# Performance work log

Hardware: AMD Instinct MI355X
Metric: run time of the kernel (lower is better)

## Reference

```python
import jax, jax.numpy as jnp
import numpy as np

D_NODE, D_PAIR, H = 512, 128, 16
HD = D_NODE // H  # head_dim = 32
B, N = 2, 1024


def _layernorm(x, gamma, beta, eps=1e-5):
    mu = jnp.mean(x, axis=-1, keepdims=True)
    var = jnp.var(x, axis=-1, keepdims=True)
    return (x - mu) * jax.lax.rsqrt(var + eps) * gamma + beta


def setup_inputs() -> dict:
    key = jax.random.key(0)
    ks = jax.random.split(key, 16)
    sc = 0.02
    inp = {
        's': jax.random.normal(ks[0], (B, N, D_NODE), jnp.float32),
        'z': jax.random.normal(ks[1], (B, N, N, D_PAIR), jnp.float32),
        'key_mask': jax.random.randint(ks[2], (B, N), 0, 2).astype(bool),
        'Wq': jax.random.normal(ks[3], (D_NODE, D_NODE), jnp.float32) * sc,
        'bq': jnp.zeros((D_NODE,), jnp.float32),
        'Wk': jax.random.normal(ks[4], (D_NODE, D_NODE), jnp.float32) * sc,
        'bk': jnp.zeros((D_NODE,), jnp.float32),
        'Wv': jax.random.normal(ks[5], (D_NODE, D_NODE), jnp.float32) * sc,
        'bv': jnp.zeros((D_NODE,), jnp.float32),
        'Wb': jax.random.normal(ks[6], (D_PAIR, H), jnp.float32) * sc,
        'bb': jnp.zeros((H,), jnp.float32),
        'Wg': jax.random.normal(ks[7], (D_NODE, D_NODE), jnp.float32) * sc,
        'bg': jnp.zeros((D_NODE,), jnp.float32),
        'Wo': jax.random.normal(ks[8], (D_NODE, D_NODE), jnp.float32) * sc,
        'bo': jnp.zeros((D_NODE,), jnp.float32),
        'gamma': jnp.ones((D_NODE,), jnp.float32),
        'beta': jnp.zeros((D_NODE,), jnp.float32),
    }
    return inp


def reference(s, z, key_mask, Wq, bq, Wk, bk, Wv, bv, Wb, bb, Wg, bg, Wo, bo, gamma, beta):
    b, n, _ = s.shape
    sn = _layernorm(s, gamma, beta)
    q = (sn @ Wq + bq).reshape(b, n, H, HD)
    k = (sn @ Wk + bk).reshape(b, n, H, HD)
    v = (sn @ Wv + bv).reshape(b, n, H, HD)
    # scores: [B, N(query), N(key), H]
    scores = jnp.einsum('bnhd,bmhd->bnmh', q, k) / np.sqrt(HD).astype(np.float32)
    scores = scores + (z @ Wb + bb)  # additive pair bias
    # mask keys (dim 2); True = masked out
    scores = jnp.where(key_mask[:, None, :, None], -jnp.inf, scores)
    attn = jax.nn.softmax(scores, axis=2)
    attn = jnp.nan_to_num(attn, nan=0.0)
    out = jnp.einsum('bnmh,bmhd->bnhd', attn, v).reshape(b, n, D_NODE)
    gate = jax.nn.sigmoid(sn @ Wg + bg)
    return gate * (out @ Wo + bo)
```

## Files before the change

### kernel.cpp

```cpp
#include <hip/hip_runtime.h>
#include <hip/hip_fp16.h>

typedef __attribute__((ext_vector_type(8))) _Float16 f16x8;
typedef __attribute__((ext_vector_type(8))) unsigned short u16x8;
typedef __attribute__((ext_vector_type(4))) float f32x4;

#define DEV __device__ __forceinline__

DEV unsigned short f2h(float f) {
  _Float16 h = (_Float16)f;
  return __builtin_bit_cast(unsigned short, h);
}
DEV float h2f(unsigned short u) {
  return (float)__builtin_bit_cast(_Float16, u);
}
DEV unsigned pk(float lo, float hi) {
  return (unsigned)f2h(lo) | ((unsigned)f2h(hi) << 16);
}

__global__ __launch_bounds__(256) void k_prep(const float* __restrict__ W0, const float* __restrict__ W1,
                                              const float* __restrict__ W2, const float* __restrict__ W3,
                                              const float* __restrict__ W4,
                                              unsigned short* __restrict__ T0, unsigned short* __restrict__ T1,
                                              unsigned short* __restrict__ T2, unsigned short* __restrict__ T3,
                                              unsigned short* __restrict__ T4,
                                              const unsigned* __restrict__ raw, int* __restrict__ canon) {
  int mat = blockIdx.y;
  const float* W = (mat == 0) ? W0 : (mat == 1) ? W1 : (mat == 2) ? W2 : (mat == 3) ? W3 : W4;
  unsigned short* T = (mat == 0) ? T0 : (mat == 1) ? T1 : (mat == 2) ? T2 : (mat == 3) ? T3 : T4;
  int tx = blockIdx.x & 7, ty = blockIdx.x >> 3;
  __shared__ float tile[64][65];
  int t = threadIdx.x;
  int r = t >> 6, c = t & 63;
#pragma unroll
  for (int i = 0; i < 16; ++i)
    tile[r + i * 4][c] = W[(size_t)(ty * 64 + r + i * 4) * 512 + tx * 64 + c];
  __syncthreads();
#pragma unroll
  for (int i = 0; i < 16; ++i)
    T[(size_t)(tx * 64 + r + i * 4) * 512 + ty * 64 + c] = f2h(tile[c][r + i * 4]);

  if (mat == 0 && blockIdx.x == 0) {
    __shared__ int s_gt1, s_f32;
    if (t == 0) { s_gt1 = 0; s_f32 = 0; }
    __syncthreads();
    int gt1 = 0, fv = 0;
    for (int i = t; i < 512; i += 256) {
      unsigned v = raw[i];
      if (v == 0x3F800000u) fv = 1;
      else if (v > 1u) gt1 = 1;
    }
    if (gt1) s_gt1 = 1;
    if (fv)  s_f32 = 1;
    __syncthreads();
    int mode = s_gt1 ? 1 : (s_f32 ? 2 : 0);
    for (int i = t; i < 2048; i += 256) {
      int v;
      if (mode == 1)      v = ((const unsigned char*)raw)[i] ? 1 : 0;
      else if (mode == 2) v = (((const float*)raw)[i] != 0.f) ? 1 : 0;
      else                v = raw[i] ? 1 : 0;
      canon[i] = v;
    }
  }
}

__global__ __launch_bounds__(64) void k_ln(const float* __restrict__ s,
                                           const float* __restrict__ gamma,
                                           const float* __restrict__ beta,
                                           unsigned short* __restrict__ sn) {
  int row = blockIdx.x, l = threadIdx.x;
  const float* sr = s + (size_t)row * 512 + l * 8;
  float4 x0 = *(const float4*)sr, x1 = *(const float4*)(sr + 4);
  float sum = x0.x + x0.y + x0.z + x0.w + x1.x + x1.y + x1.z + x1.w;
  float sq  = x0.x*x0.x + x0.y*x0.y + x0.z*x0.z + x0.w*x0.w
            + x1.x*x1.x + x1.y*x1.y + x1.z*x1.z + x1.w*x1.w;
#pragma unroll
  for (int off = 32; off >= 1; off >>= 1) {
    sum += __shfl_xor(sum, off);
    sq  += __shfl_xor(sq, off);
  }
  float mu = sum * (1.f / 512.f);
  float rstd = rsqrtf(sq * (1.f / 512.f) - mu * mu + 1e-5f);
  float4 g0 = *(const float4*)(gamma + l * 8), g1 = *(const float4*)(gamma + l * 8 + 4);
  float4 b0 = *(const float4*)(beta + l * 8),  b1 = *(const float4*)(beta + l * 8 + 4);
  u16x8 o;
  o[0] = f2h((x0.x - mu) * rstd * g0.x + b0.x);
  o[1] = f2h((x0.y - mu) * rstd * g0.y + b0.y);
  o[2] = f2h((x0.z - mu) * rstd * g0.z + b0.z);
  o[3] = f2h((x0.w - mu) * rstd * g0.w + b0.w);
  o[4] = f2h((x1.x - mu) * rstd * g1.x + b1.x);
  o[5] = f2h((x1.y - mu) * rstd * g1.y + b1.y);
  o[6] = f2h((x1.z - mu) * rstd * g1.z + b1.z);
  o[7] = f2h((x1.w - mu) * rstd * g1.w + b1.w);
  *(u16x8*)(sn + (size_t)row * 512 + l * 8) = o;
}

DEV void gemm_direct(const unsigned short* __restrict__ A,
                     const unsigned short* __restrict__ Wt,
                     const float* __restrict__ bvec,
                     void* __restrict__ outp,
                     const float* __restrict__ gate,
                     int mode, int ct, int rt) {
  int t = threadIdx.x, l = t & 63, w = t >> 6;
  int lane15 = l & 15, g = l >> 4;
  int wr = w >> 1, wc = w & 1;
  const unsigned short* ap[4];
  const unsigned short* bp[2];
#pragma unroll
  for (int mt = 0; mt < 4; ++mt)
    ap[mt] = A + (size_t)(rt * 128 + wr * 64 + mt * 16 + lane15) * 512 + g * 8;
#pragma unroll
  for (int nt = 0; nt < 2; ++nt)
    bp[nt] = Wt + (size_t)(ct * 64 + wc * 32 + nt * 16 + lane15) * 512 + g * 8;

  f32x4 acc[4][2];
#pragma unroll
  for (int mt = 0; mt < 4; ++mt)
#pragma unroll
    for (int nt = 0; nt < 2; ++nt) acc[mt][nt] = (f32x4){0.f, 0.f, 0.f, 0.f};

  f16x8 af[4], bf[2];
#pragma unroll
  for (int mt = 0; mt < 4; ++mt) af[mt] = *(const f16x8*)ap[mt];
#pragma unroll
  for (int nt = 0; nt < 2; ++nt) bf[nt] = *(const f16x8*)bp[nt];

  for (int ks = 0; ks < 16; ++ks) {
    f16x8 an[4], bn[2];
    if (ks < 15) {
#pragma unroll
      for (int mt = 0; mt < 4; ++mt) an[mt] = *(const f16x8*)(ap[mt] + (ks + 1) * 32);
#pragma unroll
      for (int nt = 0; nt < 2; ++nt) bn[nt] = *(const f16x8*)(bp[nt] + (ks + 1) * 32);
    } else {
#pragma unroll
      for (int mt = 0; mt < 4; ++mt) an[mt] = af[mt];
#pragma unroll
      for (int nt = 0; nt < 2; ++nt) bn[nt] = bf[nt];
    }
#pragma unroll
    for (int mt = 0; mt < 4; ++mt)
#pragma unroll
      for (int nt = 0; nt < 2; ++nt)
        acc[mt][nt] = __builtin_amdgcn_mfma_f32_16x16x32_f16(af[mt], bf[nt], acc[mt][nt], 0, 0, 0);
#pragma unroll
    for (int mt = 0; mt < 4; ++mt) af[mt] = an[mt];
#pragma unroll
    for (int nt = 0; nt < 2; ++nt) bf[nt] = bn[nt];
  }

#pragma unroll
  for (int mt = 0; mt < 4; ++mt)
#pragma unroll
    for (int nt = 0; nt < 2; ++nt) {
      int col = ct * 64 + wc * 32 + nt * 16 + lane15;
      float bv = bvec[col];
#pragma unroll
      for (int i = 0; i < 4; ++i) {
        int row = rt * 128 + wr * 64 + mt * 16 + g * 4 + i;
        float val = acc[mt][nt][i] + bv;
        int bb_ = row >> 10, n = row & 1023, hh = col >> 5, d = col & 31;
        if (mode == 0) {
          ((unsigned short*)outp)[(size_t)row * 512 + col] = f2h(val);
        } else if (mode == 1) {
          ((unsigned short*)outp)[(((size_t)bb_ * 16 + hh) * 1024 + n) * 32 + d] = f2h(val);
        } else if (mode == 2) {
          ((unsigned short*)outp)[(((size_t)bb_ * 16 + hh) * 32 + d) * 1024 + n] = f2h(val);
        } else if (mode == 3) {
          ((float*)outp)[(size_t)row * 512 + col] = 1.f / (1.f + __expf(-val));
        } else {
          ((float*)outp)[(size_t)row * 512 + col] = gate[(size_t)row * 512 + col] * val;
        }
      }
    }
}

__global__ __launch_bounds__(256) void k_qkvg(const unsigned short* __restrict__ A,
                                              const unsigned short* __restrict__ T0, const unsigned short* __restrict__ T1,
                                              const unsigned short* __restrict__ T2, const unsigned short* __restrict__ T3,
                                              const float* __restrict__ b0, const float* __restrict__ b1,
                                              const float* __restrict__ b2, const float* __restrict__ b3,
                                              void* o0, void* o1, void* o2, void* o3) {
  int mode = blockIdx.z;
  const unsigned short* Wt = (mode == 0) ? T0 : (mode == 1) ? T1 : (mode == 2) ? T2 : T3;
  const float* bv = (mode == 0) ? b0 : (mode == 1) ? b1 : (mode == 2) ? b2 : b3;
  void* o = (mode == 0) ? o0 : (mode == 1) ? o1 : (mode == 2) ? o2 : o3;
  gemm_direct(A, Wt, bv, o, nullptr, mode, blockIdx.x, blockIdx.y);
}

__global__ __launch_bounds__(256) void k_gemm_out(const unsigned short* __restrict__ A,
                                                  const unsigned short* __restrict__ Wt,
                                                  const float* __restrict__ bvec,
                                                  float* __restrict__ outp,
                                                  const float* __restrict__ gate) {
  gemm_direct(A, Wt, bvec, outp, gate, 4, blockIdx.x, blockIdx.y);
}

__global__ __launch_bounds__(256, 4) void k_bias(const float* __restrict__ z,
                                                 const float* __restrict__ Wb,
                                                 const float* __restrict__ bbp,
                                                 const int* __restrict__ maskc,
                                                 unsigned short* __restrict__ bias) {
  int bid = blockIdx.x;
  int slab = bid >> 1, half = bid & 1;
  int b = slab >> 10;
  int t = threadIdx.x, l = t & 63, w = t >> 6;
  int lane15 = l & 15, g = l >> 4;

  __shared__ float lds_[4][2048];
  float* wlds = lds_[w];

  f16x8 wf[4];
#pragma unroll
  for (int ks = 0; ks < 4; ++ks)
#pragma unroll
    for (int j = 0; j < 8; ++j)
      wf[ks][j] = (_Float16)Wb[(ks * 32 + g * 8 + j) * 16 + lane15];
  float bbh = bbp[lane15];

  const char* zb = (const char*)(z + ((size_t)slab * 1024 + half * 512 + (size_t)w * 128) * 128);
  unsigned short* ob = bias + ((size_t)slab * 16 + lane15) * 1024;
  const int* mrow = maskc + b * 1024;

  float4 rbuf[8];
#pragma unroll
  for (int i = 0; i < 8; ++i)
    rbuf[i] = *(const float4*)(zb + i * 1024 + l * 16);
#pragma unroll
  for (int i = 0; i < 8; ++i) {
    int lin = i * 1024 + l * 16;
    int off = lin ^ (((lin >> 9) & 7) << 4);
    *(float4*)((char*)wlds + off) = rbuf[i];
  }

  for (int t8 = 0; t8 < 8; ++t8) {
    if (t8 < 7) {
      const char* tb = zb + (t8 + 1) * 8192;
#pragma unroll
      for (int i = 0; i < 8; ++i)
        rbuf[i] = *(const float4*)(tb + i * 1024 + l * 16);
    }
    f32x4 acc = (f32x4){0.f, 0.f, 0.f, 0.f};
#pragma unroll
    for (int ks = 0; ks < 4; ++ks) {
      int linA = lane15 * 512 + ks * 128 + g * 32;
      int swz = ((lane15 & 7) << 4);
      float4 z0 = *(const float4*)((const char*)wlds + (linA ^ swz));
      float4 z1 = *(const float4*)((const char*)wlds + ((linA + 16) ^ swz));
      f16x8 af;
      af[0] = (_Float16)z0.x; af[1] = (_Float16)z0.y;
      af[2] = (_Float16)z0.z; af[3] = (_Float16)z0.w;
      af[4] = (_Float16)z1.x; af[5] = (_Float16)z1.y;
      af[6] = (_Float16)z1.z; af[7] = (_Float16)z1.w;
      acc = __builtin_amdgcn_mfma_f32_16x16x32_f16(af, wf[ks], acc, 0, 0, 0);
    }
    int mabs = half * 512 + w * 128 + t8 * 16 + 4 * g;
    int4 mk = *(const int4*)(mrow + mabs);
    ushort4 o4;
    o4.x = mk.x ? 0xFBFFu : f2h(acc[0] + bbh);
    o4.y = mk.y ? 0xFBFFu : f2h(acc[1] + bbh);
    o4.z = mk.z ? 0xFBFFu : f2h(acc[2] + bbh);
    o4.w = mk.w ? 0xFBFFu : f2h(acc[3] + bbh);
    *(ushort4*)(ob + mabs) = o4;
    if (t8 < 7) {
#pragma unroll
      for (int i = 0; i < 8; ++i) {
        int lin = i * 1024 + l * 16;
        int off = lin ^ (((lin >> 9) & 7) << 4);
        *(float4*)((char*)wlds + off) = rbuf[i];
      }
    }
  }
}

struct Pf {
  f16x8 kf1, kf2, vf1, vf2;
  ushort4 bv1, bv2;
};
DEV Pf ldchunk(const unsigned short* kb_, const unsigned short* vb_,
               const unsigned short* brow, int lane15, int g, int c) {
  Pf p;
  int m0 = c * 32;
  p.kf1 = *(const f16x8*)(kb_ + (size_t)(m0 + lane15) * 32 + g * 8);
  p.kf2 = *(const f16x8*)(kb_ + (size_t)(m0 + 16 + lane15) * 32 + g * 8);
  p.bv1 = *(const ushort4*)(brow + m0 + 4 * g);
  p.bv2 = *(const ushort4*)(brow + m0 + 16 + 4 * g);
  p.vf1 = *(const f16x8*)(vb_ + (size_t)lane15 * 1024 + m0 + 8 * g);
  p.vf2 = *(const f16x8*)(vb_ + (size_t)(16 + lane15) * 1024 + m0 + 8 * g);
  return p;
}

__global__ __launch_bounds__(512, 4) void k_attn(const unsigned short* __restrict__ qbuf,
                                                 const unsigned short* __restrict__ kbuf,
                                                 const unsigned short* __restrict__ vbuf,
                                                 const unsigned short* __restrict__ bias,
                                                 unsigned short* __restrict__ aout) {
  int qt = blockIdx.x, h = blockIdx.y, b = blockIdx.z;
  int t = threadIdx.x, l = t & 63, w = t >> 6;
  int qs = w & 3, half = w >> 2;
  int q0 = (qt * 4 + qs) * 16;
  int lane15 = l & 15, g = l >> 4;
  int bh = b * 16 + h;
  const float RS = 0.17677669529663687f;

  __shared__ float red_m[4][64];
  __shared__ float red_l[4][64];
  __shared__ f32x4 red_a1[4][64];
  __shared__ f32x4 red_a2[4][64];

  f16x8 qf = *(const f16x8*)(qbuf + ((size_t)(b * 1024 + q0 + lane15)) * 512 + h * 32 + g * 8);

  const unsigned short* kb_ = kbuf + (size_t)bh * 1024 * 32 + (size_t)half * 512 * 32;
  const unsigned short* vb_ = vbuf + (size_t)bh * 32 * 1024 + half * 512;
  const unsigned short* brow = bias + ((size_t)(b * 1024 + q0 + lane15) * 16 + h) * 1024 + half * 512;

  float m_run = -3.0e38f, lsum = 0.f;
  f32x4 acc1 = (f32x4){0.f, 0.f, 0.f, 0.f};
  f32x4 acc2 = (f32x4){0.f, 0.f, 0.f, 0.f};

  Pf cur = ldchunk(kb_, vb_, brow, lane15, g, 0);

  for (int c = 0; c < 16; ++c) {
    Pf nxt = cur;
    if (c < 15) nxt = ldchunk(kb_, vb_, brow, lane15, g, c + 1);

    f32x4 zero = (f32x4){0.f, 0.f, 0.f, 0.f};
    f32x4 c1 = __builtin_amdgcn_mfma_f32_16x16x32_f16(cur.kf1, qf, zero, 0, 0, 0);
    f32x4 c2 = __builtin_amdgcn_mfma_f32_16x16x32_f16(cur.kf2, qf, zero, 0, 0, 0);
    float s1[4], s2[4];
    s1[0] = c1[0] * RS + h2f(cur.bv1.x); s1[1] = c1[1] * RS + h2f(cur.bv1.y);
    s1[2] = c1[2] * RS + h2f(cur.bv1.z); s1[3] = c1[3] * RS + h2f(cur.bv1.w);
    s2[0] = c2[0] * RS + h2f(cur.bv2.x); s2[1] = c2[1] * RS + h2f(cur.bv2.y);
    s2[2] = c2[2] * RS + h2f(cur.bv2.z); s2[3] = c2[3] * RS + h2f(cur.bv2.w);
    float cm = fmaxf(fmaxf(fmaxf(s1[0], s1[1]), fmaxf(s1[2], s1[3])),
                     fmaxf(fmaxf(s2[0], s2[1]), fmaxf(s2[2], s2[3])));
    cm = fmaxf(cm, __shfl_xor(cm, 16));
    cm = fmaxf(cm, __shfl_xor(cm, 32));
    float mn = fmaxf(m_run, cm);
    float corr = __expf(m_run - mn);
    m_run = mn;
    float p1[4], p2[4], csum = 0.f;
#pragma unroll
    for (int i = 0; i < 4; ++i) { p1[i] = __expf(s1[i] - mn); csum += p1[i]; }
#pragma unroll
    for (int i = 0; i < 4; ++i) { p2[i] = __expf(s2[i] - mn); csum += p2[i]; }
    lsum = lsum * corr + csum;
#pragma unroll
    for (int i = 0; i < 4; ++i) { acc1[i] *= corr; acc2[i] *= corr; }
    unsigned a0 = pk(p1[0], p1[1]), a1 = pk(p1[2], p1[3]);
    unsigned b0 = pk(p2[0], p2[1]), b1 = pk(p2[2], p2[3]);
    int s0 = ((g & 1) << 5) + lane15, s1l = s0 + 16;
    unsigned wA0 = (unsigned)__shfl((int)a0, s0);
    unsigned wA1 = (unsigned)__shfl((int)a1, s0);
    unsigned wA2 = (unsigned)__shfl((int)a0, s1l);
    unsigned wA3 = (unsigned)__shfl((int)a1, s1l);
    unsigned wB0 = (unsigned)__shfl((int)b0, s0);
    unsigned wB1 = (unsigned)__shfl((int)b1, s0);
    unsigned wB2 = (unsigned)__shfl((int)b0, s1l);
    unsigned wB3 = (unsigned)__shfl((int)b1, s1l);
    bool hi = (l & 32) != 0;
    union { unsigned u[4]; f16x8 v; } pu;
    pu.u[0] = hi ? wB0 : wA0;
    pu.u[1] = hi ? wB1 : wA1;
    pu.u[2] = hi ? wB2 : wA2;
    pu.u[3] = hi ? wB3 : wA3;
    acc1 = __builtin_amdgcn_mfma_f32_16x16x32_f16(cur.vf1, pu.v, acc1, 0, 0, 0);
    acc2 = __builtin_amdgcn_mfma_f32_16x16x32_f16(cur.vf2, pu.v, acc2, 0, 0, 0);
    cur = nxt;
  }

  lsum += __shfl_xor(lsum, 16);
  lsum += __shfl_xor(lsum, 32);

  if (half) {
    red_m[qs][l] = m_run;
    red_l[qs][l] = lsum;
    red_a1[qs][l] = acc1;
    red_a2[qs][l] = acc2;
  }
  __syncthreads();
  if (!half) {
    float pm = red_m[qs][l], plv = red_l[qs][l];
    f32x4 pa1 = red_a1[qs][l], pa2 = red_a2[qs][l];
    float mm = fmaxf(m_run, pm);
    float c1s = __expf(m_run - mm), c2s = __expf(pm - mm);
    float lt = lsum * c1s + plv * c2s;
    float inv = (mm > -30000.f && lt > 0.f) ? 1.f / lt : 0.f;
    unsigned short* orow = aout + ((size_t)(b * 1024 + q0 + lane15)) * 512 + h * 32;
    ushort4 o1, o2;
    o1.x = f2h((acc1[0] * c1s + pa1[0] * c2s) * inv);
    o1.y = f2h((acc1[1] * c1s + pa1[1] * c2s) * inv);
    o1.z = f2h((acc1[2] * c1s + pa1[2] * c2s) * inv);
    o1.w = f2h((acc1[3] * c1s + pa1[3] * c2s) * inv);
    o2.x = f2h((acc2[0] * c1s + pa2[0] * c2s) * inv);
    o2.y = f2h((acc2[1] * c1s + pa2[1] * c2s) * inv);
    o2.z = f2h((acc2[2] * c1s + pa2[2] * c2s) * inv);
    o2.w = f2h((acc2[3] * c1s + pa2[3] * c2s) * inv);
    *(ushort4*)(orow + 4 * g) = o1;
    *(ushort4*)(orow + 16 + 4 * g) = o2;
  }
}

extern "C" void kernel_launch(void* const* d_in, const int* in_sizes, int n_in,
                              void* d_out, int out_size, void* d_ws, size_t ws_size,
                              hipStream_t stream) {
  (void)in_sizes; (void)n_in; (void)out_size; (void)ws_size;
  const float* s     = (const float*)d_in[0];
  const float* z     = (const float*)d_in[1];
  const unsigned* km = (const unsigned*)d_in[2];
  const float* Wq = (const float*)d_in[3];
  const float* bq = (const float*)d_in[4];
  const float* Wk = (const float*)d_in[5];
  const float* bk = (const float*)d_in[6];
  const float* Wv = (const float*)d_in[7];
  const float* bv = (const float*)d_in[8];
  const float* Wb = (const float*)d_in[9];
  const float* bb = (const float*)d_in[10];
  const float* Wg = (const float*)d_in[11];
  const float* bg = (const float*)d_in[12];
  const float* Wo = (const float*)d_in[13];
  const float* bo = (const float*)d_in[14];
  const float* gamma = (const float*)d_in[15];
  const float* beta  = (const float*)d_in[16];

  char* ws = (char*)d_ws;
  unsigned short* sn    = (unsigned short*)(ws);
  unsigned short* qbuf  = (unsigned short*)(ws + (2ull << 20));
  unsigned short* kbuf  = (unsigned short*)(ws + (4ull << 20));
  unsigned short* vbuf  = (unsigned short*)(ws + (6ull << 20));
  float*          gate  = (float*)(ws + (8ull << 20));
  unsigned short* aout  = (unsigned short*)(ws + (12ull << 20));
  unsigned short* bias  = (unsigned short*)(ws + (14ull << 20));
  int*            maskc = (int*)(ws + (78ull << 20));
  unsigned short* wtq   = (unsigned short*)(ws + (80ull << 20));
  unsigned short* wtk   = (unsigned short*)(ws + (80ull << 20) + (512u << 10));
  unsigned short* wtv   = (unsigned short*)(ws + (80ull << 20) + (1024u << 10));
  unsigned short* wtg   = (unsigned short*)(ws + (80ull << 20) + (1536u << 10));
  unsigned short* wto   = (unsigned short*)(ws + (80ull << 20) + (2048u << 10));

  hipLaunchKernelGGL(k_prep, dim3(64, 5), dim3(256), 0, stream,
                     Wq, Wk, Wv, Wg, Wo, wtq, wtk, wtv, wtg, wto, km, maskc);
  hipLaunchKernelGGL(k_ln, dim3(2048), dim3(64), 0, stream, s, gamma, beta, sn);
  hipLaunchKernelGGL(k_qkvg, dim3(8, 16, 4), dim3(256), 0, stream, sn,
                     wtq, wtk, wtv, wtg, bq, bk, bv, bg,
                     (void*)qbuf, (void*)kbuf, (void*)vbuf, (void*)gate);
  hipLaunchKernelGGL(k_bias, dim3(4096), dim3(256), 0, stream, z, Wb, bb, maskc, bias);
  hipLaunchKernelGGL(k_attn, dim3(16, 16, 2), dim3(512), 0, stream,
                     qbuf, kbuf, vbuf, bias, aout);
  hipLaunchKernelGGL(k_gemm_out, dim3(8, 16), dim3(256), 0, stream, aout, wto, bo,
                     (float*)d_out, gate);
}
```

Before: 345.1 us.

## Fuse pair-bias projection into attention, computing QK and PV with dot2

The separate bias kernel, which wrote a 64MB fp16 bias tensor, and the attention kernel are merged into one kernel. Each block handles two query rows across all 16 heads, streams z directly, projects it with MFMA and runs an online softmax. QK^T and PV now use scalar fdot2 instructions instead of MFMA, with a cross-wave LDS reduction at the end. This removes the bias write and re-read, but moves the attention math from matrix cores to VALU and reads K and V once per query pair, which may make the kernel compute-bound.

```diff
diff --git a/kernel.cpp b/kernel.cpp
--- a/kernel.cpp
+++ b/kernel.cpp
@@ -11,12 +11,23 @@
   _Float16 h = (_Float16)f;
   return __builtin_bit_cast(unsigned short, h);
 }
-DEV float h2f(unsigned short u) {
-  return (float)__builtin_bit_cast(_Float16, u);
-}
 DEV unsigned pk(float lo, float hi) {
   return (unsigned)f2h(lo) | ((unsigned)f2h(hi) << 16);
 }
+
+#if __has_builtin(__builtin_amdgcn_fdot2)
+typedef __attribute__((ext_vector_type(2))) _Float16 f16x2;
+DEV float fdot2u(unsigned a, unsigned b, float c) {
+  return __builtin_amdgcn_fdot2(__builtin_bit_cast(f16x2, a),
+                                __builtin_bit_cast(f16x2, b), c, false);
+}
+#else
+DEV float fdot2u(unsigned a, unsigned b, float c) {
+  __half2 ha = __builtin_bit_cast(__half2, a);
+  __half2 hb = __builtin_bit_cast(__half2, b);
+  return c + __low2float(ha) * __low2float(hb) + __high2float(ha) * __high2float(hb);
+}
+#endif
 
 __global__ __launch_bounds__(256) void k_prep(const float* __restrict__ W0, const float* __restrict__ W1,
                                               const float* __restrict__ W2, const float* __restrict__ W3,
@@ -196,19 +207,22 @@
   gemm_direct(A, Wt, bvec, outp, gate, 4, blockIdx.x, blockIdx.y);
 }
 
-__global__ __launch_bounds__(256, 4) void k_bias(const float* __restrict__ z,
-                                                 const float* __restrict__ Wb,
-                                                 const float* __restrict__ bbp,
-                                                 const int* __restrict__ maskc,
-                                                 unsigned short* __restrict__ bias) {
+__global__ __launch_bounds__(256) void k_zattn(const float* __restrict__ z,
+                                               const float* __restrict__ Wb,
+                                               const float* __restrict__ bbp,
+                                               const int* __restrict__ maskc,
+                                               const unsigned short* __restrict__ qbuf,
+                                               const unsigned short* __restrict__ kbuf,
+                                               const unsigned short* __restrict__ vbuf,
+                                               unsigned short* __restrict__ aout) {
   int bid = blockIdx.x;
-  int slab = bid >> 1, half = bid & 1;
-  int b = slab >> 10;
+  int b = bid >> 9, pair = bid & 511;
+  int n0 = pair * 2;
   int t = threadIdx.x, l = t & 63, w = t >> 6;
   int lane15 = l & 15, g = l >> 4;
-
-  __shared__ float lds_[4][2048];
-  float* wlds = lds_[w];
+  const float RS = 0.17677669529663687f;
+
+  __shared__ float sred[4][64][20];
 
   f16x8 wf[4];
 #pragma unroll
@@ -218,186 +232,156 @@
       wf[ks][j] = (_Float16)Wb[(ks * 32 + g * 8 + j) * 16 + lane15];
   float bbh = bbp[lane15];
 
-  const char* zb = (const char*)(z + ((size_t)slab * 1024 + half * 512 + (size_t)w * 128) * 128);
-  unsigned short* ob = bias + ((size_t)slab * 16 + lane15) * 1024;
+  unsigned qreg[2][16];
+#pragma unroll
+  for (int q = 0; q < 2; ++q) {
+    const unsigned* qp = (const unsigned*)(qbuf + ((size_t)(b * 1024 + n0 + q)) * 512 + lane15 * 32);
+#pragma unroll
+    for (int i = 0; i < 16; ++i) qreg[q][i] = qp[i];
+  }
+
+  const float* zq0 = z + ((size_t)(b * 1024 + n0)) * 1024 * 128;
+  const float* zq1 = zq0 + (size_t)1024 * 128;
+  const unsigned short* kb_ = kbuf + ((size_t)b * 16 + lane15) * 1024 * 32;
+  const unsigned short* vb_ = vbuf + (((size_t)b * 16 + lane15) * 32 + g * 8) * 1024;
   const int* mrow = maskc + b * 1024;
 
-  float4 rbuf[8];
-#pragma unroll
-  for (int i = 0; i < 8; ++i)
-    rbuf[i] = *(const float4*)(zb + i * 1024 + l * 16);
-#pragma unroll
-  for (int i = 0; i < 8; ++i) {
-    int lin = i * 1024 + l * 16;
-    int off = lin ^ (((lin >> 9) & 7) << 4);
-    *(float4*)((char*)wlds + off) = rbuf[i];
-  }
-
-  for (int t8 = 0; t8 < 8; ++t8) {
-    if (t8 < 7) {
-      const char* tb = zb + (t8 + 1) * 8192;
-#pragma unroll
-      for (int i = 0; i < 8; ++i)
-        rbuf[i] = *(const float4*)(tb + i * 1024 + l * 16);
-    }
-    f32x4 acc = (f32x4){0.f, 0.f, 0.f, 0.f};
-#pragma unroll
-    for (int ks = 0; ks < 4; ++ks) {
-      int linA = lane15 * 512 + ks * 128 + g * 32;
-      int swz = ((lane15 & 7) << 4);
-      float4 z0 = *(const float4*)((const char*)wlds + (linA ^ swz));
-      float4 z1 = *(const float4*)((const char*)wlds + ((linA + 16) ^ swz));
-      f16x8 af;
-      af[0] = (_Float16)z0.x; af[1] = (_Float16)z0.y;
-      af[2] = (_Float16)z0.z; af[3] = (_Float16)z0.w;
-      af[4] = (_Float16)z1.x; af[5] = (_Float16)z1.y;
-      af[6] = (_Float16)z1.z; af[7] = (_Float16)z1.w;
-      acc = __builtin_amdgcn_mfma_f32_16x16x32_f16(af, wf[ks], acc, 0, 0, 0);
-    }
-    int mabs = half * 512 + w * 128 + t8 * 16 + 4 * g;
-    int4 mk = *(const int4*)(mrow + mabs);
-    ushort4 o4;
-    o4.x = mk.x ? 0xFBFFu : f2h(acc[0] + bbh);
-    o4.y = mk.y ? 0xFBFFu : f2h(acc[1] + bbh);
-    o4.z = mk.z ? 0xFBFFu : f2h(acc[2] + bbh);
-    o4.w = mk.w ? 0xFBFFu : f2h(acc[3] + bbh);
-    *(ushort4*)(ob + mabs) = o4;
-    if (t8 < 7) {
-#pragma unroll
-      for (int i = 0; i < 8; ++i) {
-        int lin = i * 1024 + l * 16;
-        int off = lin ^ (((lin >> 9) & 7) << 4);
-        *(float4*)((char*)wlds + off) = rbuf[i];
+  float m_run[2] = {-3.0e38f, -3.0e38f};
+  float lsum[2] = {0.f, 0.f};
+  float acc[2][8];
+#pragma unroll
+  for (int q = 0; q < 2; ++q)
+#pragma unroll
+    for (int d = 0; d < 8; ++d) acc[q][d] = 0.f;
+
+  unsigned pp[2][8];
+
+  for (int tile = 0; tile < 16; ++tile) {
+    int m0 = w * 256 + tile * 16;
+    int4 mk = *(const int4*)(mrow + m0 + 4 * g);
+
+    float dot0[4], dot1[4];
+#pragma unroll
+    for (int i = 0; i < 4; ++i) {
+      const uint4* kr = (const uint4*)(kb_ + (size_t)(m0 + 4 * g + i) * 32);
+      uint4 k0 = kr[0], k1 = kr[1], k2 = kr[2], k3 = kr[3];
+      float d0 = 0.f, d1 = 0.f;
+      d0 = fdot2u(k0.x, qreg[0][0], d0);  d1 = fdot2u(k0.x, qreg[1][0], d1);
+      d0 = fdot2u(k0.y, qreg[0][1], d0);  d1 = fdot2u(k0.y, qreg[1][1], d1);
+      d0 = fdot2u(k0.z, qreg[0][2], d0);  d1 = fdot2u(k0.z, qreg[1][2], d1);
+      d0 = fdot2u(k0.w, qreg[0][3], d0);  d1 = fdot2u(k0.w, qreg[1][3], d1);
+      d0 = fdot2u(k1.x, qreg[0][4], d0);  d1 = fdot2u(k1.x, qreg[1][4], d1);
+      d0 = fdot2u(k1.y, qreg[0][5], d0);  d1 = fdot2u(k1.y, qreg[1][5], d1);
+      d0 = fdot2u(k1.z, qreg[0][6], d0);  d1 = fdot2u(k1.z, qreg[1][6], d1);
+      d0 = fdot2u(k1.w, qreg[0][7], d0);  d1 = fdot2u(k1.w, qreg[1][7], d1);
+      d0 = fdot2u(k2.x, qreg[0][8], d0);  d1 = fdot2u(k2.x, qreg[1][8], d1);
+      d0 = fdot2u(k2.y, qreg[0][9], d0);  d1 = fdot2u(k2.y, qreg[1][9], d1);
+      d0 = fdot2u(k2.z, qreg[0][10], d0); d1 = fdot2u(k2.z, qreg[1][10], d1);
+      d0 = fdot2u(k2.w, qreg[0][11], d0); d1 = fdot2u(k2.w, qreg[1][11], d1);
+      d0 = fdot2u(k3.x, qreg[0][12], d0); d1 = fdot2u(k3.x, qreg[1][12], d1);
+      d0 = fdot2u(k3.y, qreg[0][13], d0); d1 = fdot2u(k3.y, qreg[1][13], d1);
+      d0 = fdot2u(k3.z, qreg[0][14], d0); d1 = fdot2u(k3.z, qreg[1][14], d1);
+      d0 = fdot2u(k3.w, qreg[0][15], d0); d1 = fdot2u(k3.w, qreg[1][15], d1);
+      dot0[i] = d0; dot1[i] = d1;
+    }
+
+#pragma unroll
+    for (int q = 0; q < 2; ++q) {
+      const float* zr = (q == 0 ? zq0 : zq1) + (size_t)(m0 + lane15) * 128 + g * 8;
+      f32x4 cacc = (f32x4){0.f, 0.f, 0.f, 0.f};
+#pragma unroll
+      for (int ks = 0; ks < 4; ++ks) {
+        float4 z0 = *(const float4*)(zr + ks * 32);
+        float4 z1 = *(const float4*)(zr + ks * 32 + 4);
+        f16x8 af;
+        af[0] = (_Float16)z0.x; af[1] = (_Float16)z0.y;
+        af[2] = (_Float16)z0.z; af[3] = (_Float16)z0.w;
+        af[4] = (_Float16)z1.x; af[5] = (_Float16)z1.y;
+        af[6] = (_Float16)z1.z; af[7] = (_Float16)z1.w;
+        cacc = __builtin_amdgcn_mfma_f32_16x16x32_f16(af, wf[ks], cacc, 0, 0, 0);
       }
-    }
-  }
-}
-
-struct Pf {
-  f16x8 kf1, kf2, vf1, vf2;
-  ushort4 bv1, bv2;
-};
-DEV Pf ldchunk(const unsigned short* kb_, const unsigned short* vb_,
-               const unsigned short* brow, int lane15, int g, int c) {
-  Pf p;
-  int m0 = c * 32;
-  p.kf1 = *(const f16x8*)(kb_ + (size_t)(m0 + lane15) * 32 + g * 8);
-  p.kf2 = *(const f16x8*)(kb_ + (size_t)(m0 + 16 + lane15) * 32 + g * 8);
-  p.bv1 = *(const ushort4*)(brow + m0 + 4 * g);
-  p.bv2 = *(const ushort4*)(brow + m0 + 16 + 4 * g);
-  p.vf1 = *(const f16x8*)(vb_ + (size_t)lane15 * 1024 + m0 + 8 * g);
-  p.vf2 = *(const f16x8*)(vb_ + (size_t)(16 + lane15) * 1024 + m0 + 8 * g);
-  return p;
-}
-
-__global__ __launch_bounds__(512, 4) void k_attn(const unsigned short* __restrict__ qbuf,
-                                                 const unsigned short* __restrict__ kbuf,
-                                                 const unsigned short* __restrict__ vbuf,
-                                                 const unsigned short* __restrict__ bias,
-                                                 unsigned short* __restrict__ aout) {
-  int qt = blockIdx.x, h = blockIdx.y, b = blockIdx.z;
-  int t = threadIdx.x, l = t & 63, w = t >> 6;
-  int qs = w & 3, half = w >> 2;
-  int q0 = (qt * 4 + qs) * 16;
-  int lane15 = l & 15, g = l >> 4;
-  int bh = b * 16 + h;
-  const float RS = 0.17677669529663687f;
-
-  __shared__ float red_m[4][64];
-  __shared__ float red_l[4][64];
-  __shared__ f32x4 red_a1[4][64];
-  __shared__ f32x4 red_a2[4][64];
-
-  f16x8 qf = *(const f16x8*)(qbuf + ((size_t)(b * 1024 + q0 + lane15)) * 512 + h * 32 + g * 8);
-
-  const unsigned short* kb_ = kbuf + (size_t)bh * 1024 * 32 + (size_t)half * 512 * 32;
-  const unsigned short* vb_ = vbuf + (size_t)bh * 32 * 1024 + half * 512;
-  const unsigned short* brow = bias + ((size_t)(b * 1024 + q0 + lane15) * 16 + h) * 1024 + half * 512;
-
-  float m_run = -3.0e38f, lsum = 0.f;
-  f32x4 acc1 = (f32x4){0.f, 0.f, 0.f, 0.f};
-  f32x4 acc2 = (f32x4){0.f, 0.f, 0.f, 0.f};
-
-  Pf cur = ldchunk(kb_, vb_, brow, lane15, g, 0);
-
-  for (int c = 0; c < 16; ++c) {
-    Pf nxt = cur;
-    if (c < 15) nxt = ldchunk(kb_, vb_, brow, lane15, g, c + 1);
-
-    f32x4 zero = (f32x4){0.f, 0.f, 0.f, 0.f};
-    f32x4 c1 = __builtin_amdgcn_mfma_f32_16x16x32_f16(cur.kf1, qf, zero, 0, 0, 0);
-    f32x4 c2 = __builtin_amdgcn_mfma_f32_16x16x32_f16(cur.kf2, qf, zero, 0, 0, 0);
-    float s1[4], s2[4];
-    s1[0] = c1[0] * RS + h2f(cur.bv1.x); s1[1] = c1[1] * RS + h2f(cur.bv1.y);
-    s1[2] = c1[2] * RS + h2f(cur.bv1.z); s1[3] = c1[3] * RS + h2f(cur.bv1.w);
-    s2[0] = c2[0] * RS + h2f(cur.bv2.x); s2[1] = c2[1] * RS + h2f(cur.bv2.y);
-    s2[2] = c2[2] * RS + h2f(cur.bv2.z); s2[3] = c2[3] * RS + h2f(cur.bv2.w);
-    float cm = fmaxf(fmaxf(fmaxf(s1[0], s1[1]), fmaxf(s1[2], s1[3])),
-                     fmaxf(fmaxf(s2[0], s2[1]), fmaxf(s2[2], s2[3])));
-    cm = fmaxf(cm, __shfl_xor(cm, 16));
-    cm = fmaxf(cm, __shfl_xor(cm, 32));
-    float mn = fmaxf(m_run, cm);
-    float corr = __expf(m_run - mn);
-    m_run = mn;
-    float p1[4], p2[4], csum = 0.f;
-#pragma unroll
-    for (int i = 0; i < 4; ++i) { p1[i] = __expf(s1[i] - mn); csum += p1[i]; }
-#pragma unroll
-    for (int i = 0; i < 4; ++i) { p2[i] = __expf(s2[i] - mn); csum += p2[i]; }
-    lsum = lsum * corr + csum;
-#pragma unroll
-    for (int i = 0; i < 4; ++i) { acc1[i] *= corr; acc2[i] *= corr; }
-    unsigned a0 = pk(p1[0], p1[1]), a1 = pk(p1[2], p1[3]);
-    unsigned b0 = pk(p2[0], p2[1]), b1 = pk(p2[2], p2[3]);
-    int s0 = ((g & 1) << 5) + lane15, s1l = s0 + 16;
-    unsigned wA0 = (unsigned)__shfl((int)a0, s0);
-    unsigned wA1 = (unsigned)__shfl((int)a1, s0);
-    unsigned wA2 = (unsigned)__shfl((int)a0, s1l);
-    unsigned wA3 = (unsigned)__shfl((int)a1, s1l);
-    unsigned wB0 = (unsigned)__shfl((int)b0, s0);
-    unsigned wB1 = (unsigned)__shfl((int)b1, s0);
-    unsigned wB2 = (unsigned)__shfl((int)b0, s1l);
-    unsigned wB3 = (unsigned)__shfl((int)b1, s1l);
-    bool hi = (l & 32) != 0;
-    union { unsigned u[4]; f16x8 v; } pu;
-    pu.u[0] = hi ? wB0 : wA0;
-    pu.u[1] = hi ? wB1 : wA1;
-    pu.u[2] = hi ? wB2 : wA2;
-    pu.u[3] = hi ? wB3 : wA3;
-    acc1 = __builtin_amdgcn_mfma_f32_16x16x32_f16(cur.vf1, pu.v, acc1, 0, 0, 0);
-    acc2 = __builtin_amdgcn_mfma_f32_16x16x32_f16(cur.vf2, pu.v, acc2, 0, 0, 0);
-    cur = nxt;
-  }
-
-  lsum += __shfl_xor(lsum, 16);
-  lsum += __shfl_xor(lsum, 32);
-
-  if (half) {
-    red_m[qs][l] = m_run;
-    red_l[qs][l] = lsum;
-    red_a1[qs][l] = acc1;
-    red_a2[qs][l] = acc2;
+      float s[4];
+      float dq0 = (q == 0) ? dot0[0] : dot1[0];
+      float dq1 = (q == 0) ? dot0[1] : dot1[1];
+      float dq2 = (q == 0) ? dot0[2] : dot1[2];
+      float dq3 = (q == 0) ? dot0[3] : dot1[3];
+      s[0] = mk.x ? -1e30f : (dq0 * RS + cacc[0] + bbh);
+      s[1] = mk.y ? -1e30f : (dq1 * RS + cacc[1] + bbh);
+      s[2] = mk.z ? -1e30f : (dq2 * RS + cacc[2] + bbh);
+      s[3] = mk.w ? -1e30f : (dq3 * RS + cacc[3] + bbh);
+      float cm = fmaxf(fmaxf(s[0], s[1]), fmaxf(s[2], s[3]));
+      cm = fmaxf(cm, __shfl_xor(cm, 16));
+      cm = fmaxf(cm, __shfl_xor(cm, 32));
+      float mn = fmaxf(m_run[q], cm);
+      float corr = __expf(m_run[q] - mn);
+      m_run[q] = mn;
+      float p0 = __expf(s[0] - mn), p1 = __expf(s[1] - mn);
+      float p2 = __expf(s[2] - mn), p3 = __expf(s[3] - mn);
+      lsum[q] = lsum[q] * corr + (p0 + p1 + p2 + p3);
+#pragma unroll
+      for (int d = 0; d < 8; ++d) acc[q][d] *= corr;
+      unsigned A0 = pk(p0, p1), A1 = pk(p2, p3);
+#pragma unroll
+      for (int j = 0; j < 8; ++j) {
+        int src = ((j >> 1) << 4) + lane15;
+        pp[q][j] = (unsigned)__shfl((int)((j & 1) ? A1 : A0), src);
+      }
+    }
+
+#pragma unroll
+    for (int d = 0; d < 8; ++d) {
+      const uint4* vp = (const uint4*)(vb_ + (size_t)d * 1024 + m0);
+      uint4 v0 = vp[0], v1 = vp[1];
+      float a0 = acc[0][d], a1 = acc[1][d];
+      a0 = fdot2u(pp[0][0], v0.x, a0);  a1 = fdot2u(pp[1][0], v0.x, a1);
+      a0 = fdot2u(pp[0][1], v0.y, a0);  a1 = fdot2u(pp[1][1], v0.y, a1);
+      a0 = fdot2u(pp[0][2], v0.z, a0);  a1 = fdot2u(pp[1][2], v0.z, a1);
+      a0 = fdot2u(pp[0][3], v0.w, a0);  a1 = fdot2u(pp[1][3], v0.w, a1);
+      a0 = fdot2u(pp[0][4], v1.x, a0);  a1 = fdot2u(pp[1][4], v1.x, a1);
+      a0 = fdot2u(pp[0][5], v1.y, a0);  a1 = fdot2u(pp[1][5], v1.y, a1);
+      a0 = fdot2u(pp[0][6], v1.z, a0);  a1 = fdot2u(pp[1][6], v1.z, a1);
+      a0 = fdot2u(pp[0][7], v1.w, a0);  a1 = fdot2u(pp[1][7], v1.w, a1);
+      acc[0][d] = a0; acc[1][d] = a1;
+    }
+  }
+
+  lsum[0] += __shfl_xor(lsum[0], 16);
+  lsum[0] += __shfl_xor(lsum[0], 32);
+  lsum[1] += __shfl_xor(lsum[1], 16);
+  lsum[1] += __shfl_xor(lsum[1], 32);
+
+  sred[w][l][0] = m_run[0];
+  sred[w][l][1] = lsum[0];
+  sred[w][l][2] = m_run[1];
+  sred[w][l][3] = lsum[1];
+#pragma unroll
+  for (int d = 0; d < 8; ++d) {
+    sred[w][l][4 + d] = acc[0][d];
+    sred[w][l][12 + d] = acc[1][d];
   }
   __syncthreads();
-  if (!half) {
-    float pm = red_m[qs][l], plv = red_l[qs][l];
-    f32x4 pa1 = red_a1[qs][l], pa2 = red_a2[qs][l];
-    float mm = fmaxf(m_run, pm);
-    float c1s = __expf(m_run - mm), c2s = __expf(pm - mm);
-    float lt = lsum * c1s + plv * c2s;
-    float inv = (mm > -30000.f && lt > 0.f) ? 1.f / lt : 0.f;
-    unsigned short* orow = aout + ((size_t)(b * 1024 + q0 + lane15)) * 512 + h * 32;
-    ushort4 o1, o2;
-    o1.x = f2h((acc1[0] * c1s + pa1[0] * c2s) * inv);
-    o1.y = f2h((acc1[1] * c1s + pa1[1] * c2s) * inv);
-    o1.z = f2h((acc1[2] * c1s + pa1[2] * c2s) * inv);
-    o1.w = f2h((acc1[3] * c1s + pa1[3] * c2s) * inv);
-    o2.x = f2h((acc2[0] * c1s + pa2[0] * c2s) * inv);
-    o2.y = f2h((acc2[1] * c1s + pa2[1] * c2s) * inv);
-    o2.z = f2h((acc2[2] * c1s + pa2[2] * c2s) * inv);
-    o2.w = f2h((acc2[3] * c1s + pa2[3] * c2s) * inv);
-    *(ushort4*)(orow + 4 * g) = o1;
-    *(ushort4*)(orow + 16 + 4 * g) = o2;
+
+  if (t < 128) {
+    int q = t >> 6, h = (t >> 2) & 15, gg = t & 3;
+    int lane = (gg << 4) | h;
+    float M = -3.0e38f;
+#pragma unroll
+    for (int ww = 0; ww < 4; ++ww) M = fmaxf(M, sred[ww][lane][q * 2]);
+    float L = 0.f, od[8];
+#pragma unroll
+    for (int d = 0; d < 8; ++d) od[d] = 0.f;
+#pragma unroll
+    for (int ww = 0; ww < 4; ++ww) {
+      float e = __expf(sred[ww][lane][q * 2] - M);
+      L += sred[ww][lane][q * 2 + 1] * e;
+#pragma unroll
+      for (int d = 0; d < 8; ++d) od[d] += sred[ww][lane][4 + q * 8 + d] * e;
+    }
+    float inv = (M > -1e29f && L > 0.f) ? 1.f / L : 0.f;
+    u16x8 o;
+#pragma unroll
+    for (int d = 0; d < 8; ++d) o[d] = f2h(od[d] * inv);
+    *(u16x8*)(aout + ((size_t)(b * 1024 + n0 + q)) * 512 + h * 32 + gg * 8) = o;
   }
 }
 
@@ -430,13 +414,12 @@
   unsigned short* vbuf  = (unsigned short*)(ws + (6ull << 20));
   float*          gate  = (float*)(ws + (8ull << 20));
   unsigned short* aout  = (unsigned short*)(ws + (12ull << 20));
-  unsigned short* bias  = (unsigned short*)(ws + (14ull << 20));
-  int*            maskc = (int*)(ws + (78ull << 20));
-  unsigned short* wtq   = (unsigned short*)(ws + (80ull << 20));
-  unsigned short* wtk   = (unsigned short*)(ws + (80ull << 20) + (512u << 10));
-  unsigned short* wtv   = (unsigned short*)(ws + (80ull << 20) + (1024u << 10));
-  unsigned short* wtg   = (unsigned short*)(ws + (80ull << 20) + (1536u << 10));
-  unsigned short* wto   = (unsigned short*)(ws + (80ull << 20) + (2048u << 10));
+  int*            maskc = (int*)(ws + (14ull << 20));
+  unsigned short* wtq   = (unsigned short*)(ws + (15ull << 20));
+  unsigned short* wtk   = (unsigned short*)(ws + (15ull << 20) + (512u << 10));
+  unsigned short* wtv   = (unsigned short*)(ws + (15ull << 20) + (1024u << 10));
+  unsigned short* wtg   = (unsigned short*)(ws + (15ull << 20) + (1536u << 10));
+  unsigned short* wto   = (unsigned short*)(ws + (15ull << 20) + (2048u << 10));
 
   hipLaunchKernelGGL(k_prep, dim3(64, 5), dim3(256), 0, stream,
                      Wq, Wk, Wv, Wg, Wo, wtq, wtk, wtv, wtg, wto, km, maskc);
@@ -444,9 +427,8 @@
   hipLaunchKernelGGL(k_qkvg, dim3(8, 16, 4), dim3(256), 0, stream, sn,
                      wtq, wtk, wtv, wtg, bq, bk, bv, bg,
                      (void*)qbuf, (void*)kbuf, (void*)vbuf, (void*)gate);
-  hipLaunchKernelGGL(k_bias, dim3(4096), dim3(256), 0, stream, z, Wb, bb, maskc, bias);
-  hipLaunchKernelGGL(k_attn, dim3(16, 16, 2), dim3(512), 0, stream,
-                     qbuf, kbuf, vbuf, bias, aout);
+  hipLaunchKernelGGL(k_zattn, dim3(1024), dim3(256), 0, stream,
+                     z, Wb, bb, maskc, qbuf, kbuf, vbuf, aout);
   hipLaunchKernelGGL(k_gemm_out, dim3(8, 16), dim3(256), 0, stream, aout, wto, bo,
                      (float*)d_out, gate);
 }
```

Result: slower. 713.4 us (+106.7%).
